# Kernel tuning notes

Measured on AMD Instinct MI355X. Metric: run time of the kernel, lower is better.

The kernel has to match this reference:

```python
import jax, jax.numpy as jnp
import numpy as np

N_NODES = 100000
N_EDGES = 3200000
IN_CH = 128
HID = 64
OUT_CH = 10
N_GRAPHS = 128


def setup_inputs() -> dict:
    key = jax.random.key(0)
    ks = jax.random.split(key, 10)
    w = lambda k, shape: jax.random.normal(k, shape, jnp.float32) * 0.05
    return {
        "x": jax.random.normal(ks[0], (N_NODES, IN_CH), jnp.float32),
        "edge_index": jax.random.randint(ks[1], (2, N_EDGES), 0, N_NODES),
        "batch": jnp.sort(jax.random.randint(ks[2], (N_NODES,), 0, N_GRAPHS)),
        "num_graphs": N_GRAPHS,
        # conv 0: MLP([128, 64, 64])
        "w1_0": w(ks[3], (IN_CH, HID)), "b1_0": jnp.zeros((HID,), jnp.float32),
        "w2_0": w(ks[4], (HID, HID)), "b2_0": jnp.zeros((HID,), jnp.float32),
        # convs 1..4: MLP([64, 64, 64]) each, stacked on leading axis
        "ws1": w(ks[5], (4, HID, HID)), "bs1": jnp.zeros((4, HID), jnp.float32),
        "ws2": w(ks[6], (4, HID, HID)), "bs2": jnp.zeros((4, HID), jnp.float32),
        # final MLP([64, 64, out_channels], dropout=0.5) -- dropout is identity at inference
        "mlp_w1": w(ks[7], (HID, HID)), "mlp_b1": jnp.zeros((HID,), jnp.float32),
        "mlp_w2": w(ks[8], (HID, OUT_CH)), "mlp_b2": jnp.zeros((OUT_CH,), jnp.float32),
    }


def _gin_conv(x, src, dst, w1, b1, w2, b2):
    # GINConv(train_eps=False): h = MLP((1+0)*x + sum_{j in N(i)} x_j)
    aggr = jax.ops.segment_sum(x[src], dst, num_segments=x.shape[0])  # [N, C]
    h = x + aggr
    h = jax.nn.relu(h @ w1 + b1) @ w2 + b2  # MLP([C,64,64], norm=None)
    return jax.nn.relu(h)  # outer x.relu() in forward


def reference(x, edge_index, batch, num_graphs, w1_0, b1_0, w2_0, b2_0,
              ws1, bs1, ws2, bs2, mlp_w1, mlp_b1, mlp_w2, mlp_b2):
    src, dst = edge_index[0], edge_index[1]
    x = _gin_conv(x, src, dst, w1_0, b1_0, w2_0, b2_0)
    for i in range(4):  # fixed 5-layer stack, layers 1..4 share shapes
        x = _gin_conv(x, src, dst, ws1[i], bs1[i], ws2[i], bs2[i])
    g = jax.ops.segment_sum(x, batch, num_segments=num_graphs)  # global_add_pool -> [G, 64]
    h = jax.nn.relu(g @ mlp_w1 + mlp_b1)  # dropout(0.5) identity in eval mode
    return h @ mlp_w2 + mlp_b2  # [G, out_channels]
```

## Files before the change

kernel.cpp:

```cpp
#include <hip/hip_runtime.h>
#include <hip/hip_bf16.h>
#include <stdint.h>

constexpr int N_NODES  = 100000;
constexpr int N_EDGES  = 3200000;
constexpr int IN_CH    = 128;
constexpr int HID      = 64;
constexpr int OUT_CH   = 10;
constexpr int N_GRAPHS = 128;
constexpr int ROW_CAP  = 72;

constexpr int NGRP   = 256;
constexpr int GRP_SZ = (N_NODES + NGRP - 1) / NGRP;

constexpr int NBLK  = 256;
constexpr int CHUNK = N_EDGES / NBLK;

typedef __attribute__((ext_vector_type(8))) short short8;
typedef __attribute__((ext_vector_type(4))) float f32x4;
typedef __attribute__((ext_vector_type(2))) float f32x2;

__device__ inline unsigned int f2bf(float f) {
    unsigned int u = __float_as_uint(f);
    u += 0x7FFFu + ((u >> 16) & 1u);
    return u >> 16;
}
__device__ inline void splitbf(float f, unsigned short& hi, unsigned short& lo) {
    unsigned int uh = f2bf(f);
    hi = (unsigned short)uh;
    float fh = __uint_as_float(uh << 16);
    lo = (unsigned short)f2bf(f - fh);
}

__device__ inline unsigned int f2fp8(float f) {
    unsigned int su = (__float_as_uint(f) >> 24) & 0x80u;
    float a = fabsf(f);
    if (a < 0.015625f) return su;
    a = fminf(a, 448.0f);
    unsigned int u = __float_as_uint(a);
    u += 0x7FFFFu + ((u >> 20) & 1u);
    unsigned int e8 = (u >> 23) - 120u;
    return su | (e8 << 3) | ((u >> 20) & 7u);
}

__device__ inline int block_incl_scan(int v, int* wsums) {
    int t = threadIdx.x, lane = t & 63, wid = t >> 6;
    int incl = v;
    #pragma unroll
    for (int off = 1; off < 64; off <<= 1) {
        int tv = __shfl_up(incl, off, 64);
        if (lane >= off) incl += tv;
    }
    if (lane == 63) wsums[wid] = incl;
    __syncthreads();
    int wpre = 0;
    #pragma unroll
    for (int w = 0; w < 4; ++w) if (w < wid) wpre += wsums[w];
    return wpre + incl;
}

__global__ __launch_bounds__(256)
void hist_kernel(const int* __restrict__ dst, int* __restrict__ hist) {
    __shared__ int lh[NGRP];
    lh[threadIdx.x] = 0;
    __syncthreads();
    int base = blockIdx.x * CHUNK;
    for (int j = threadIdx.x; j < CHUNK; j += 256) {
        int d = __builtin_nontemporal_load(dst + base + j);
        atomicAdd(&lh[d / GRP_SZ], 1);
    }
    __syncthreads();
    hist[blockIdx.x * NGRP + threadIdx.x] = lh[threadIdx.x];
}

__global__ __launch_bounds__(256)
void scan_bucket_kernel(const int* __restrict__ hist, int* __restrict__ partial,
                        int* __restrict__ total) {
    __shared__ int wsums[4];
    int g = blockIdx.x;
    int t = threadIdx.x;
    int v = hist[t * NGRP + g];
    int incl = block_incl_scan(v, wsums);
    partial[t * NGRP + g] = incl - v;
    if (t == 255) total[g] = incl;
}

__global__ __launch_bounds__(256)
void scan_total_kernel(const int* __restrict__ total, int* __restrict__ bstart) {
    __shared__ int wsums[4];
    int t = threadIdx.x;
    int v = total[t];
    int incl = block_incl_scan(v, wsums);
    bstart[t] = incl - v;
    if (t == 255) bstart[NGRP] = incl;
}

__global__ __launch_bounds__(256)
void compact_kernel(const int* __restrict__ src, const int* __restrict__ dst,
                    const int* __restrict__ partial, const int* __restrict__ bstart,
                    unsigned long long* __restrict__ rec) {
    __shared__ int lcnt[NGRP];
    __shared__ int lbase[NGRP];
    lcnt[threadIdx.x] = 0;
    lbase[threadIdx.x] = bstart[threadIdx.x] + partial[blockIdx.x * NGRP + threadIdx.x];
    __syncthreads();
    int base = blockIdx.x * CHUNK;
    for (int j = threadIdx.x; j < CHUNK; j += 256) {
        int d = __builtin_nontemporal_load(dst + base + j);
        int s = __builtin_nontemporal_load(src + base + j);
        int bk = d / GRP_SZ;
        int p = atomicAdd(&lcnt[bk], 1);
        rec[(size_t)lbase[bk] + p] = (unsigned)d | ((unsigned long long)(unsigned)s << 32);
    }
}

__global__ __launch_bounds__(256)
void scatterC_kernel(const unsigned long long* __restrict__ rec, const int* __restrict__ bstart,
                     int* __restrict__ cnt, int* __restrict__ col) {
    __shared__ int lcnt[GRP_SZ];
    int b = blockIdx.x;
    int lo = b * GRP_SZ;
    for (int i = threadIdx.x; i < GRP_SZ; i += 256) lcnt[i] = 0;
    __syncthreads();
    int s0 = bstart[b], s1 = bstart[b + 1];
    for (int i = s0 + threadIdx.x; i < s1; i += 256) {
        unsigned long long r = __builtin_nontemporal_load(rec + i);
        int d = (int)(r & 0xFFFFFFFFu);
        int s = (int)(r >> 32);
        int p = atomicAdd(&lcnt[d - lo], 1);
        if (p < ROW_CAP) col[(size_t)d * ROW_CAP + p] = s;
    }
    __syncthreads();
    for (int i = threadIdx.x; i < GRP_SZ; i += 256) {
        int v = lo + i;
        if (v < N_NODES) cnt[v] = lcnt[i];
    }
}

__global__ __launch_bounds__(256)
void gemm0_mfma_kernel(const float* __restrict__ x, const float* __restrict__ w1,
                       unsigned char* __restrict__ y) {
    __shared__ unsigned short wt_hi[128 * 64];
    __shared__ unsigned short wt_lo[128 * 64];
    int tid = threadIdx.x;

    #pragma unroll
    for (int e = 0; e < 32; ++e) {
        int idx = tid + e * 256;
        int k = idx >> 6, c = idx & 63;
        int pos = c * 128 + (((k >> 3) ^ (c & 7)) << 3) + (k & 7);
        unsigned short h16, l16;
        splitbf(w1[idx], h16, l16);
        wt_hi[pos] = h16; wt_lo[pos] = l16;
    }
    __syncthreads();

    int wid = tid >> 6, lane = tid & 63;
    int r = lane & 15, kb = lane >> 4;
    int row = blockIdx.x * 64 + wid * 16 + r;
    int rowc = min(row, N_NODES - 1);

    short8 ahi[4], alo[4];
    #pragma unroll
    for (int kap = 0; kap < 4; ++kap) {
        const float4* xp = reinterpret_cast<const float4*>(x + (size_t)rowc * 128 + kap * 32 + kb * 8);
        float4 v0 = xp[0], v1 = xp[1];
        float tv[8] = {v0.x, v0.y, v0.z, v0.w, v1.x, v1.y, v1.z, v1.w};
        #pragma unroll
        for (int j = 0; j < 8; ++j) {
            unsigned short h16, l16;
            splitbf(tv[j], h16, l16);
            ahi[kap][j] = (short)h16; alo[kap][j] = (short)l16;
        }
    }

    f32x4 acc[4];
    #pragma unroll
    for (int n = 0; n < 4; ++n) acc[n] = (f32x4)0.0f;
    #pragma unroll
    for (int n = 0; n < 4; ++n) {
        int c = n * 16 + r;
        #pragma unroll
        for (int kap = 0; kap < 4; ++kap) {
            int pos = c * 128 + ((((kap << 2) + kb) ^ (c & 7)) << 3);
            short8 bh = *reinterpret_cast<const short8*>(wt_hi + pos);
            short8 bl = *reinterpret_cast<const short8*>(wt_lo + pos);
            acc[n] = __builtin_amdgcn_mfma_f32_16x16x32_bf16(ahi[kap], bh, acc[n], 0, 0, 0);
            acc[n] = __builtin_amdgcn_mfma_f32_16x16x32_bf16(alo[kap], bh, acc[n], 0, 0, 0);
            acc[n] = __builtin_amdgcn_mfma_f32_16x16x32_bf16(ahi[kap], bl, acc[n], 0, 0, 0);
        }
    }

    #pragma unroll
    for (int n = 0; n < 4; ++n) {
        int col = n * 16 + r;
        #pragma unroll
        for (int j = 0; j < 4; ++j) {
            int orow = blockIdx.x * 64 + wid * 16 + kb * 4 + j;
            if (orow < N_NODES)
                y[(size_t)orow * 64 + col] = (unsigned char)f2fp8(acc[n][j]);
        }
    }
}

__global__ __launch_bounds__(256)
void aggregate_kernel(const unsigned char* __restrict__ y, const int* __restrict__ cnt,
                      const int* __restrict__ col, float* __restrict__ h) {
    int wave = blockIdx.x * 4 + (threadIdx.x >> 6);
    int lane = threadIdx.x & 63;
    int g = lane >> 3;
    int i = lane & 7;
    const uint2* ybase = reinterpret_cast<const uint2*>(y);

    int cn = min(cnt[wave], ROW_CAP);
    const int* crow = col + (size_t)wave * ROW_CAP;

    float acc[8];
    #pragma unroll
    for (int k = 0; k < 8; ++k) acc[k] = 0.0f;

    auto addrow = [&](uint2 v) {
        f32x2 p0 = __builtin_amdgcn_cvt_pk_f32_fp8((int)v.x, false);
        f32x2 p1 = __builtin_amdgcn_cvt_pk_f32_fp8((int)v.x, true);
        f32x2 p2 = __builtin_amdgcn_cvt_pk_f32_fp8((int)v.y, false);
        f32x2 p3 = __builtin_amdgcn_cvt_pk_f32_fp8((int)v.y, true);
        acc[0] += p0.x; acc[1] += p0.y;
        acc[2] += p1.x; acc[3] += p1.y;
        acc[4] += p2.x; acc[5] += p2.y;
        acc[6] += p3.x; acc[7] += p3.y;
    };

    {
        int c0 = (g == 0) ? wave : N_NODES;
        addrow(ybase[(size_t)c0 * 8 + i]);
    }

    for (int e = 0; e < cn; e += 32) {
        int i0 = e + g, i1 = e + 8 + g, i2 = e + 16 + g, i3 = e + 24 + g;
        int c0 = (i0 < cn) ? __builtin_nontemporal_load(crow + i0) : N_NODES;
        int c1 = (i1 < cn) ? __builtin_nontemporal_load(crow + i1) : N_NODES;
        int c2 = (i2 < cn) ? __builtin_nontemporal_load(crow + i2) : N_NODES;
        int c3 = (i3 < cn) ? __builtin_nontemporal_load(crow + i3) : N_NODES;
        uint2 v0 = ybase[(size_t)c0 * 8 + i];
        uint2 v1 = ybase[(size_t)c1 * 8 + i];
        uint2 v2 = ybase[(size_t)c2 * 8 + i];
        uint2 v3 = ybase[(size_t)c3 * 8 + i];
        addrow(v0);
        addrow(v1);
        addrow(v2);
        addrow(v3);
    }

    #pragma unroll
    for (int off = 8; off < 64; off <<= 1) {
        #pragma unroll
        for (int k = 0; k < 8; ++k) acc[k] += __shfl_xor(acc[k], off, 64);
    }

    if (g == 0) {
        float4* hp = reinterpret_cast<float4*>(h + (size_t)wave * 64 + i * 8);
        float4 o0, o1;
        o0.x = acc[0]; o0.y = acc[1]; o0.z = acc[2]; o0.w = acc[3];
        o1.x = acc[4]; o1.y = acc[5]; o1.z = acc[6]; o1.w = acc[7];
        hp[0] = o0; hp[1] = o1;
    }
}

template <bool LAST>
__global__ __launch_bounds__(256)
void mlp_mfma_kernel(const float* __restrict__ h, const float* __restrict__ b1,
                     const float* __restrict__ w2, const float* __restrict__ b2,
                     const float* __restrict__ w1n, unsigned char* __restrict__ ynext,
                     float* __restrict__ uout) {
    __shared__ unsigned short w2t_hi[64 * 64];
    __shared__ unsigned short w2t_lo[64 * 64];
    __shared__ unsigned short w1t_hi[64 * 64];
    __shared__ unsigned short w1t_lo[64 * 64];
    __shared__ unsigned short tt_hi[64 * 64];
    __shared__ unsigned short tt_lo[64 * 64];
    int tid = threadIdx.x;

    #pragma unroll
    for (int e = 0; e < 16; ++e) {
        int idx = tid + e * 256;
        int k = idx >> 6, c = idx & 63;
        int pos = c * 64 + (((k >> 3) ^ (c & 7)) << 3) + (k & 7);
        unsigned short h16, l16;
        splitbf(w2[idx], h16, l16);
        w2t_hi[pos] = h16; w2t_lo[pos] = l16;
        if (!LAST) {
            splitbf(w1n[idx], h16, l16);
            w1t_hi[pos] = h16; w1t_lo[pos] = l16;
        }
    }
    __syncthreads();

    int wid = tid >> 6, lane = tid & 63;
    int r = lane & 15, kb = lane >> 4;
    int row = blockIdx.x * 64 + wid * 16 + r;
    int rowc = min(row, N_NODES - 1);

    short8 ahi[2], alo[2];
    #pragma unroll
    for (int kap = 0; kap < 2; ++kap) {
        const float4* hp = reinterpret_cast<const float4*>(h + (size_t)rowc * 64 + kap * 32 + kb * 8);
        const float4* bp = reinterpret_cast<const float4*>(b1 + kap * 32 + kb * 8);
        float4 h0 = hp[0], h1 = hp[1];
        float4 b0 = bp[0], b1v = bp[1];
        float tv[8] = {fmaxf(h0.x + b0.x, 0.f), fmaxf(h0.y + b0.y, 0.f),
                       fmaxf(h0.z + b0.z, 0.f), fmaxf(h0.w + b0.w, 0.f),
                       fmaxf(h1.x + b1v.x, 0.f), fmaxf(h1.y + b1v.y, 0.f),
                       fmaxf(h1.z + b1v.z, 0.f), fmaxf(h1.w + b1v.w, 0.f)};
        #pragma unroll
        for (int j = 0; j < 8; ++j) {
            unsigned short h16, l16;
            splitbf(tv[j], h16, l16);
            ahi[kap][j] = (short)h16; alo[kap][j] = (short)l16;
        }
    }

    f32x4 acc[4];
    #pragma unroll
    for (int n = 0; n < 4; ++n) acc[n] = (f32x4)0.0f;
    #pragma unroll
    for (int n = 0; n < 4; ++n) {
        int c = n * 16 + r;
        #pragma unroll
        for (int kap = 0; kap < 2; ++kap) {
            int pos = c * 64 + ((((kap << 2) + kb) ^ (c & 7)) << 3);
            short8 bh = *reinterpret_cast<const short8*>(w2t_hi + pos);
            short8 bl = *reinterpret_cast<const short8*>(w2t_lo + pos);
            acc[n] = __builtin_amdgcn_mfma_f32_16x16x32_bf16(ahi[kap], bh, acc[n], 0, 0, 0);
            acc[n] = __builtin_amdgcn_mfma_f32_16x16x32_bf16(alo[kap], bh, acc[n], 0, 0, 0);
            acc[n] = __builtin_amdgcn_mfma_f32_16x16x32_bf16(ahi[kap], bl, acc[n], 0, 0, 0);
        }
    }

    #pragma unroll
    for (int n = 0; n < 4; ++n) {
        float b2v = b2[n * 16 + r];
        #pragma unroll
        for (int j = 0; j < 4; ++j) acc[n][j] = fmaxf(acc[n][j] + b2v, 0.f);
    }

    if constexpr (LAST) {
        #pragma unroll
        for (int n = 0; n < 4; ++n) {
            int col = n * 16 + r;
            #pragma unroll
            for (int j = 0; j < 4; ++j) {
                int orow = blockIdx.x * 64 + wid * 16 + kb * 4 + j;
                if (orow < N_NODES) uout[(size_t)orow * 64 + col] = acc[n][j];
            }
        }
    } else {
        #pragma unroll
        for (int n = 0; n < 4; ++n) {
            int col = n * 16 + r;
            #pragma unroll
            for (int j = 0; j < 4; ++j) {
                int trow = wid * 16 + kb * 4 + j;
                int pos = trow * 64 + (((col >> 3) ^ (trow & 7)) << 3) + (col & 7);
                unsigned short h16, l16;
                splitbf(acc[n][j], h16, l16);
                tt_hi[pos] = h16; tt_lo[pos] = l16;
            }
        }
        __syncthreads();

        short8 uhi[2], ulo[2];
        #pragma unroll
        for (int kap = 0; kap < 2; ++kap) {
            int trow = wid * 16 + r;
            int pos = trow * 64 + ((((kap << 2) + kb) ^ (trow & 7)) << 3);
            uhi[kap] = *reinterpret_cast<const short8*>(tt_hi + pos);
            ulo[kap] = *reinterpret_cast<const short8*>(tt_lo + pos);
        }

        f32x4 acc2[4];
        #pragma unroll
        for (int n = 0; n < 4; ++n) acc2[n] = (f32x4)0.0f;
        #pragma unroll
        for (int n = 0; n < 4; ++n) {
            int c = n * 16 + r;
            #pragma unroll
            for (int kap = 0; kap < 2; ++kap) {
                int pos = c * 64 + ((((kap << 2) + kb) ^ (c & 7)) << 3);
                short8 bh = *reinterpret_cast<const short8*>(w1t_hi + pos);
                short8 bl = *reinterpret_cast<const short8*>(w1t_lo + pos);
                acc2[n] = __builtin_amdgcn_mfma_f32_16x16x32_bf16(uhi[kap], bh, acc2[n], 0, 0, 0);
                acc2[n] = __builtin_amdgcn_mfma_f32_16x16x32_bf16(ulo[kap], bh, acc2[n], 0, 0, 0);
                acc2[n] = __builtin_amdgcn_mfma_f32_16x16x32_bf16(uhi[kap], bl, acc2[n], 0, 0, 0);
            }
        }

        #pragma unroll
        for (int n = 0; n < 4; ++n) {
            int col = n * 16 + r;
            #pragma unroll
            for (int j = 0; j < 4; ++j) {
                int orow = blockIdx.x * 64 + wid * 16 + kb * 4 + j;
                if (orow < N_NODES)
                    ynext[(size_t)orow * 64 + col] = (unsigned char)f2fp8(acc2[n][j]);
            }
        }
    }
}

__global__ __launch_bounds__(256)
void pool_kernel(const float* __restrict__ x, const int* __restrict__ batch,
                 float* __restrict__ g, int n) {
    const int NW = 1024;
    int w = blockIdx.x * (blockDim.x >> 6) + (threadIdx.x >> 6);
    int lane = threadIdx.x & 63;
    int per = (n + NW - 1) / NW;
    int r0 = w * per;
    int r1 = min(n, r0 + per);
    if (r0 >= r1) return;
    int cur = batch[r0];
    float acc = 0.0f;
    for (int r = r0; r < r1; ++r) {
        int b = batch[r];
        if (b != cur) {
            atomicAdd(&g[(size_t)cur * 64 + lane], acc);
            acc = 0.0f;
            cur = b;
        }
        acc += x[(size_t)r * 64 + lane];
    }
    atomicAdd(&g[(size_t)cur * 64 + lane], acc);
}

__global__ __launch_bounds__(128)
void final_mlp_kernel(const float* __restrict__ g, const float* __restrict__ w1,
                      const float* __restrict__ b1, const float* __restrict__ w2,
                      const float* __restrict__ b2, float* __restrict__ out, int G) {
    int row = blockIdx.x * blockDim.x + threadIdx.x;
    if (row >= G) return;
    float hr[64];
    const float4* gp = reinterpret_cast<const float4*>(g + (size_t)row * 64);
    #pragma unroll
    for (int i = 0; i < 16; ++i) {
        float4 v = gp[i];
        hr[4 * i + 0] = v.x; hr[4 * i + 1] = v.y;
        hr[4 * i + 2] = v.z; hr[4 * i + 3] = v.w;
    }
    float t[64];
    #pragma unroll
    for (int c = 0; c < 64; ++c) t[c] = b1[c];
    #pragma unroll
    for (int k = 0; k < 64; ++k) {
        const float* wrow = w1 + (size_t)k * 64;
        #pragma unroll
        for (int c = 0; c < 64; ++c) t[c] = fmaf(hr[k], wrow[c], t[c]);
    }
    #pragma unroll
    for (int c = 0; c < 64; ++c) t[c] = fmaxf(t[c], 0.0f);
    #pragma unroll
    for (int o = 0; o < OUT_CH; ++o) {
        float acc = b2[o];
        #pragma unroll
        for (int k = 0; k < 64; ++k) acc = fmaf(t[k], w2[(size_t)k * OUT_CH + o], acc);
        out[(size_t)row * OUT_CH + o] = acc;
    }
}

extern "C" void kernel_launch(void* const* d_in, const int* in_sizes, int n_in,
                              void* d_out, int out_size, void* d_ws, size_t ws_size,
                              hipStream_t stream) {
    const float* x      = (const float*)d_in[0];
    const int*   ei     = (const int*)d_in[1];
    const int*   src    = ei;
    const int*   dst    = ei + N_EDGES;
    const int*   batch  = (const int*)d_in[2];
    const float* w1_0   = (const float*)d_in[4];
    const float* b1_0   = (const float*)d_in[5];
    const float* w2_0   = (const float*)d_in[6];
    const float* b2_0   = (const float*)d_in[7];
    const float* ws1    = (const float*)d_in[8];
    const float* bs1    = (const float*)d_in[9];
    const float* ws2    = (const float*)d_in[10];
    const float* bs2    = (const float*)d_in[11];
    const float* mlp_w1 = (const float*)d_in[12];
    const float* mlp_b1 = (const float*)d_in[13];
    const float* mlp_w2 = (const float*)d_in[14];
    const float* mlp_b2 = (const float*)d_in[15];
    float* out = (float*)d_out;

    uintptr_t p = (uintptr_t)d_ws;
    auto alloc = [&](size_t bytes) {
        uintptr_t cur = (p + 255) & ~(uintptr_t)255;
        p = cur + bytes;
        return (void*)cur;
    };
    int*            cnt      = (int*)alloc((size_t)N_NODES * 4);
    int*            col      = (int*)alloc((size_t)N_NODES * ROW_CAP * 4);
    float*          h        = (float*)alloc((size_t)N_NODES * 64 * 4);
    float*          u        = (float*)alloc((size_t)N_NODES * 64 * 4);
    unsigned char*  yA       = (unsigned char*)alloc((size_t)(N_NODES + 1) * 64);
    unsigned char*  yB       = (unsigned char*)alloc((size_t)(N_NODES + 1) * 64);
    float*          g        = (float*)alloc((size_t)N_GRAPHS * 64 * 4);
    int*            hist     = (int*)alloc((size_t)NBLK * NGRP * 4);
    int*            partial  = (int*)alloc((size_t)NBLK * NGRP * 4);
    int*            total    = (int*)alloc((size_t)NGRP * 4);
    int*            bstart   = (int*)alloc((size_t)(NGRP + 1) * 4);
    unsigned long long* rec  = (unsigned long long*)h;

    hipMemsetAsync(g, 0, (size_t)N_GRAPHS * 64 * 4, stream);
    hipMemsetAsync(yA + (size_t)N_NODES * 64, 0, 64, stream);
    hipMemsetAsync(yB + (size_t)N_NODES * 64, 0, 64, stream);

    hist_kernel<<<NBLK, 256, 0, stream>>>(dst, hist);
    scan_bucket_kernel<<<NGRP, 256, 0, stream>>>(hist, partial, total);
    scan_total_kernel<<<1, 256, 0, stream>>>(total, bstart);
    compact_kernel<<<NBLK, 256, 0, stream>>>(src, dst, partial, bstart, rec);
    scatterC_kernel<<<NGRP, 256, 0, stream>>>(rec, bstart, cnt, col);

    const int mfma_blocks = (N_NODES + 63) / 64;
    const int aggr_blocks = N_NODES / 4;

    gemm0_mfma_kernel<<<mfma_blocks, 256, 0, stream>>>(x, w1_0, yA);

    aggregate_kernel<<<aggr_blocks, 256, 0, stream>>>(yA, cnt, col, h);
    mlp_mfma_kernel<false><<<mfma_blocks, 256, 0, stream>>>(h, b1_0, w2_0, b2_0,
                                                            ws1, yB, nullptr);
    unsigned char* yc = yB;
    unsigned char* yn = yA;
    for (int l = 1; l <= 3; ++l) {
        aggregate_kernel<<<aggr_blocks, 256, 0, stream>>>(yc, cnt, col, h);
        mlp_mfma_kernel<false><<<mfma_blocks, 256, 0, stream>>>(
            h, bs1 + (size_t)(l - 1) * 64, ws2 + (size_t)(l - 1) * 4096,
            bs2 + (size_t)(l - 1) * 64, ws1 + (size_t)l * 4096, yn, nullptr);
        unsigned char* tmp = yc; yc = yn; yn = tmp;
    }
    aggregate_kernel<<<aggr_blocks, 256, 0, stream>>>(yc, cnt, col, h);
    mlp_mfma_kernel<true><<<mfma_blocks, 256, 0, stream>>>(
        h, bs1 + 3 * 64, ws2 + 3 * 4096, bs2 + 3 * 64, nullptr, nullptr, u);

    pool_kernel<<<256, 256, 0, stream>>>(u, batch, g, N_NODES);
    final_mlp_kernel<<<1, 128, 0, stream>>>(g, mlp_w1, mlp_b1, mlp_w2, mlp_b2, out, N_GRAPHS);
}
```

Measured before the change: 595.7 us.

## Store aggregated features as bf16 and widen CSR-build kernels to 1024 threads

The aggregate kernel now writes its per-node sums as bf16 instead of fp32, and the MLP kernel reads and unpacks bf16. This halves the traffic for the intermediate h buffer between the two kernels in every layer. Separately, the histogram, compaction and scatter kernels that build the adjacency now run 1024-thread blocks, giving more parallelism per block over the same number of blocks. The bf16 store adds rounding error on the aggregated values, and the edge record buffer is moved to alias u because h is now too small to hold it.

```diff
diff --git a/kernel.cpp b/kernel.cpp
--- a/kernel.cpp
+++ b/kernel.cpp
@@ -59,18 +59,18 @@
     return wpre + incl;
 }
 
-__global__ __launch_bounds__(256)
+__global__ __launch_bounds__(1024)
 void hist_kernel(const int* __restrict__ dst, int* __restrict__ hist) {
     __shared__ int lh[NGRP];
-    lh[threadIdx.x] = 0;
+    if (threadIdx.x < NGRP) lh[threadIdx.x] = 0;
     __syncthreads();
     int base = blockIdx.x * CHUNK;
-    for (int j = threadIdx.x; j < CHUNK; j += 256) {
+    for (int j = threadIdx.x; j < CHUNK; j += 1024) {
         int d = __builtin_nontemporal_load(dst + base + j);
         atomicAdd(&lh[d / GRP_SZ], 1);
     }
     __syncthreads();
-    hist[blockIdx.x * NGRP + threadIdx.x] = lh[threadIdx.x];
+    if (threadIdx.x < NGRP) hist[blockIdx.x * NGRP + threadIdx.x] = lh[threadIdx.x];
 }
 
 __global__ __launch_bounds__(256)
@@ -95,17 +95,19 @@
     if (t == 255) bstart[NGRP] = incl;
 }
 
-__global__ __launch_bounds__(256)
+__global__ __launch_bounds__(1024)
 void compact_kernel(const int* __restrict__ src, const int* __restrict__ dst,
                     const int* __restrict__ partial, const int* __restrict__ bstart,
                     unsigned long long* __restrict__ rec) {
     __shared__ int lcnt[NGRP];
     __shared__ int lbase[NGRP];
-    lcnt[threadIdx.x] = 0;
-    lbase[threadIdx.x] = bstart[threadIdx.x] + partial[blockIdx.x * NGRP + threadIdx.x];
+    if (threadIdx.x < NGRP) {
+        lcnt[threadIdx.x] = 0;
+        lbase[threadIdx.x] = bstart[threadIdx.x] + partial[blockIdx.x * NGRP + threadIdx.x];
+    }
     __syncthreads();
     int base = blockIdx.x * CHUNK;
-    for (int j = threadIdx.x; j < CHUNK; j += 256) {
+    for (int j = threadIdx.x; j < CHUNK; j += 1024) {
         int d = __builtin_nontemporal_load(dst + base + j);
         int s = __builtin_nontemporal_load(src + base + j);
         int bk = d / GRP_SZ;
@@ -114,16 +116,16 @@
     }
 }
 
-__global__ __launch_bounds__(256)
+__global__ __launch_bounds__(1024)
 void scatterC_kernel(const unsigned long long* __restrict__ rec, const int* __restrict__ bstart,
                      int* __restrict__ cnt, int* __restrict__ col) {
     __shared__ int lcnt[GRP_SZ];
     int b = blockIdx.x;
     int lo = b * GRP_SZ;
-    for (int i = threadIdx.x; i < GRP_SZ; i += 256) lcnt[i] = 0;
+    for (int i = threadIdx.x; i < GRP_SZ; i += 1024) lcnt[i] = 0;
     __syncthreads();
     int s0 = bstart[b], s1 = bstart[b + 1];
-    for (int i = s0 + threadIdx.x; i < s1; i += 256) {
+    for (int i = s0 + threadIdx.x; i < s1; i += 1024) {
         unsigned long long r = __builtin_nontemporal_load(rec + i);
         int d = (int)(r & 0xFFFFFFFFu);
         int s = (int)(r >> 32);
@@ -131,7 +133,7 @@
         if (p < ROW_CAP) col[(size_t)d * ROW_CAP + p] = s;
     }
     __syncthreads();
-    for (int i = threadIdx.x; i < GRP_SZ; i += 256) {
+    for (int i = threadIdx.x; i < GRP_SZ; i += 1024) {
         int v = lo + i;
         if (v < N_NODES) cnt[v] = lcnt[i];
     }
@@ -205,7 +207,7 @@
 
 __global__ __launch_bounds__(256)
 void aggregate_kernel(const unsigned char* __restrict__ y, const int* __restrict__ cnt,
-                      const int* __restrict__ col, float* __restrict__ h) {
+                      const int* __restrict__ col, unsigned short* __restrict__ h) {
     int wave = blockIdx.x * 4 + (threadIdx.x >> 6);
     int lane = threadIdx.x & 63;
     int g = lane >> 3;
@@ -258,17 +260,18 @@
     }
 
     if (g == 0) {
-        float4* hp = reinterpret_cast<float4*>(h + (size_t)wave * 64 + i * 8);
-        float4 o0, o1;
-        o0.x = acc[0]; o0.y = acc[1]; o0.z = acc[2]; o0.w = acc[3];
-        o1.x = acc[4]; o1.y = acc[5]; o1.z = acc[6]; o1.w = acc[7];
-        hp[0] = o0; hp[1] = o1;
+        uint4 ow;
+        ow.x = f2bf(acc[0]) | (f2bf(acc[1]) << 16);
+        ow.y = f2bf(acc[2]) | (f2bf(acc[3]) << 16);
+        ow.z = f2bf(acc[4]) | (f2bf(acc[5]) << 16);
+        ow.w = f2bf(acc[6]) | (f2bf(acc[7]) << 16);
+        reinterpret_cast<uint4*>(h + (size_t)wave * 64)[i] = ow;
     }
 }
 
 template <bool LAST>
 __global__ __launch_bounds__(256)
-void mlp_mfma_kernel(const float* __restrict__ h, const float* __restrict__ b1,
+void mlp_mfma_kernel(const unsigned short* __restrict__ hb, const float* __restrict__ b1,
                      const float* __restrict__ w2, const float* __restrict__ b2,
                      const float* __restrict__ w1n, unsigned char* __restrict__ ynext,
                      float* __restrict__ uout) {
@@ -303,14 +306,20 @@
     short8 ahi[2], alo[2];
     #pragma unroll
     for (int kap = 0; kap < 2; ++kap) {
-        const float4* hp = reinterpret_cast<const float4*>(h + (size_t)rowc * 64 + kap * 32 + kb * 8);
+        uint4 hv = reinterpret_cast<const uint4*>(hb + (size_t)rowc * 64)[kap * 4 + kb];
         const float4* bp = reinterpret_cast<const float4*>(b1 + kap * 32 + kb * 8);
-        float4 h0 = hp[0], h1 = hp[1];
         float4 b0 = bp[0], b1v = bp[1];
-        float tv[8] = {fmaxf(h0.x + b0.x, 0.f), fmaxf(h0.y + b0.y, 0.f),
-                       fmaxf(h0.z + b0.z, 0.f), fmaxf(h0.w + b0.w, 0.f),
-                       fmaxf(h1.x + b1v.x, 0.f), fmaxf(h1.y + b1v.y, 0.f),
-                       fmaxf(h1.z + b1v.z, 0.f), fmaxf(h1.w + b1v.w, 0.f)};
+        unsigned int hw[4] = {hv.x, hv.y, hv.z, hv.w};
+        float hvals[8];
+        #pragma unroll
+        for (int m = 0; m < 4; ++m) {
+            hvals[2 * m]     = __uint_as_float(hw[m] << 16);
+            hvals[2 * m + 1] = __uint_as_float(hw[m] & 0xFFFF0000u);
+        }
+        float tv[8] = {fmaxf(hvals[0] + b0.x, 0.f), fmaxf(hvals[1] + b0.y, 0.f),
+                       fmaxf(hvals[2] + b0.z, 0.f), fmaxf(hvals[3] + b0.w, 0.f),
+                       fmaxf(hvals[4] + b1v.x, 0.f), fmaxf(hvals[5] + b1v.y, 0.f),
+                       fmaxf(hvals[6] + b1v.z, 0.f), fmaxf(hvals[7] + b1v.w, 0.f)};
         #pragma unroll
         for (int j = 0; j < 8; ++j) {
             unsigned short h16, l16;
@@ -495,7 +504,7 @@
     };
     int*            cnt      = (int*)alloc((size_t)N_NODES * 4);
     int*            col      = (int*)alloc((size_t)N_NODES * ROW_CAP * 4);
-    float*          h        = (float*)alloc((size_t)N_NODES * 64 * 4);
+    unsigned short* h        = (unsigned short*)alloc((size_t)N_NODES * 64 * 2);
     float*          u        = (float*)alloc((size_t)N_NODES * 64 * 4);
     unsigned char*  yA       = (unsigned char*)alloc((size_t)(N_NODES + 1) * 64);
     unsigned char*  yB       = (unsigned char*)alloc((size_t)(N_NODES + 1) * 64);
@@ -504,17 +513,17 @@
     int*            partial  = (int*)alloc((size_t)NBLK * NGRP * 4);
     int*            total    = (int*)alloc((size_t)NGRP * 4);
     int*            bstart   = (int*)alloc((size_t)(NGRP + 1) * 4);
-    unsigned long long* rec  = (unsigned long long*)h;
+    unsigned long long* rec  = (unsigned long long*)u;
 
     hipMemsetAsync(g, 0, (size_t)N_GRAPHS * 64 * 4, stream);
     hipMemsetAsync(yA + (size_t)N_NODES * 64, 0, 64, stream);
     hipMemsetAsync(yB + (size_t)N_NODES * 64, 0, 64, stream);
 
-    hist_kernel<<<NBLK, 256, 0, stream>>>(dst, hist);
+    hist_kernel<<<NBLK, 1024, 0, stream>>>(dst, hist);
     scan_bucket_kernel<<<NGRP, 256, 0, stream>>>(hist, partial, total);
     scan_total_kernel<<<1, 256, 0, stream>>>(total, bstart);
-    compact_kernel<<<NBLK, 256, 0, stream>>>(src, dst, partial, bstart, rec);
-    scatterC_kernel<<<NGRP, 256, 0, stream>>>(rec, bstart, cnt, col);
+    compact_kernel<<<NBLK, 1024, 0, stream>>>(src, dst, partial, bstart, rec);
+    scatterC_kernel<<<NGRP, 1024, 0, stream>>>(rec, bstart, cnt, col);
 
     const int mfma_blocks = (N_NODES + 63) / 64;
     const int aggr_blocks = N_NODES / 4;
```

After: 569.3 us. 4.4% less time.
